# Kernel tuning notes

Measured on AMD Instinct MI355X. Metric: run time of the kernel, lower is better.

## Reference

```python
import jax, jax.numpy as jnp
import numpy as np

B, S, HID = 2, 2048, 2048
NH, HD = 16, 128
KVC, QC = 512, 1536


def _rope(x):
    # x: [B, H, S, D]; interleaved-pair rotation matching the torch view(..., D//2, 2)
    b, h, s, d = x.shape
    inv_freq = 1.0 / (10000.0 ** (jnp.arange(0, d, 2, dtype=jnp.float32) / d))  # [D/2]
    pos = jnp.arange(s, dtype=jnp.float32)
    sinusoid = pos[:, None] * inv_freq[None, :]  # [S, D/2]
    sin = jnp.sin(sinusoid)[None, None]  # [1,1,S,D/2]
    cos = jnp.cos(sinusoid)[None, None]
    xr = x.reshape(b, h, s, d // 2, 2)
    x1, x2 = xr[..., 0], xr[..., 1]
    out = jnp.stack([x1 * cos - x2 * sin, x1 * sin + x2 * cos], axis=-1)
    return out.reshape(b, h, s, d)


def setup_inputs() -> dict:
    key = jax.random.key(0)
    ks = jax.random.split(key, 14)
    def lin(k, fan_in, fan_out):
        lim = 1.0 / np.sqrt(fan_in)
        kw, kb = jax.random.split(k)
        W = jax.random.uniform(kw, (fan_in, fan_out), jnp.float32, -lim, lim)
        b = jax.random.uniform(kb, (fan_out,), jnp.float32, -lim, lim)
        return W, b
    x = jax.random.normal(ks[0], (B, S, HID), jnp.float32)
    # causal mask (positions with 0 are masked out)
    attention_mask = jnp.tril(jnp.ones((S, S), jnp.int32))[None, None]  # [1,1,S,S]
    W_dkv, b_dkv = lin(ks[1], HID, KVC)
    W_uk, b_uk = lin(ks[2], KVC, NH * HD)
    W_uv, b_uv = lin(ks[3], KVC, NH * HD)
    W_dq, b_dq = lin(ks[4], HID, QC)
    W_uq, b_uq = lin(ks[5], QC, NH * HD)
    W_o, b_o = lin(ks[6], NH * HD, HID)
    return dict(x=x, attention_mask=attention_mask,
                W_dkv=W_dkv, b_dkv=b_dkv, W_uk=W_uk, b_uk=b_uk,
                W_uv=W_uv, b_uv=b_uv, W_dq=W_dq, b_dq=b_dq,
                W_uq=W_uq, b_uq=b_uq, W_o=W_o, b_o=b_o)


def reference(x, attention_mask, W_dkv, b_dkv, W_uk, b_uk, W_uv, b_uv,
              W_dq, b_dq, W_uq, b_uq, W_o, b_o):
    b, s, _ = x.shape
    kv = x @ W_dkv + b_dkv                                   # [B,S,KVC]
    k = (kv @ W_uk + b_uk).reshape(b, s, NH, HD).transpose(0, 2, 1, 3)  # [B,H,S,D]
    v = (kv @ W_uv + b_uv).reshape(b, s, NH, HD).transpose(0, 2, 1, 3)
    q = ((x @ W_dq + b_dq) @ W_uq + b_uq).reshape(b, s, NH, HD).transpose(0, 2, 1, 3)
    q, k = _rope(q), _rope(k)
    scores = jnp.einsum('bhqd,bhkd->bhqk', q, k) / jnp.sqrt(jnp.float32(HD))
    scores = jnp.where(attention_mask == 0, jnp.float32(-1e9), scores)
    probs = jax.nn.softmax(scores, axis=-1)
    out = jnp.einsum('bhqk,bhkd->bhqd', probs, v)            # [B,H,S,D]
    out = out.transpose(0, 2, 1, 3).reshape(b, s, NH * HD)
    return out @ W_o + b_o
```

## Files before the change

### kernel.cpp

```cpp
#include <hip/hip_runtime.h>
#include <stdint.h>

typedef unsigned short u16;
typedef uint32_t u32;
typedef __attribute__((ext_vector_type(8))) short short8;
typedef __attribute__((ext_vector_type(4))) float f32x4;
typedef __attribute__((ext_vector_type(4))) u32 u32x4;
typedef __attribute__((ext_vector_type(2))) u32 u32x2;
typedef __attribute__((ext_vector_type(4))) unsigned short u16x4;

#define BS_ 4096
#define S_ 2048
#define HID_ 2048
#define KVB 32

__device__ __forceinline__ float bf2f(u16 u) { union { u32 i; float f; } v; v.i = ((u32)u) << 16; return v.f; }
__device__ __forceinline__ u16 f2bf(float f) {
  union { float f; u32 i; } v; v.f = f;
  u32 r = v.i + 0x7fffu + ((v.i >> 16) & 1u);
  return (u16)(r >> 16);
}

__device__ __forceinline__ void gload16(const void* gsrc, void* ldst) {
  __builtin_amdgcn_global_load_lds(
      (const __attribute__((address_space(1))) void*)gsrc,
      (__attribute__((address_space(3))) void*)ldst, 16, 0, 0);
}

__global__ __launch_bounds__(256) void conv_f2b(const float* __restrict__ in, u16* __restrict__ out, int n4) {
  int i = blockIdx.x * 256 + threadIdx.x;
  if (i < n4) {
    float4 v = ((const float4*)in)[i];
    u16x4 o;
    o.x = f2bf(v.x); o.y = f2bf(v.y); o.z = f2bf(v.z); o.w = f2bf(v.w);
    ((u16x4*)out)[i] = o;
  }
}

__global__ __launch_bounds__(256) void transpose_conv(const float* __restrict__ W, u16* __restrict__ WT,
                                                      int K, int N) {
  __shared__ float tile[64][65];
  const int t = threadIdx.x;
  const int kb = blockIdx.y * 64, nb = blockIdx.x * 64;
#pragma unroll
  for (int c = 0; c < 4; ++c) {
    int idx = c * 256 + t;
    int row = idx >> 4;
    int col4 = (idx & 15) * 4;
    float4 v = *(const float4*)&W[(size_t)(kb + row) * N + nb + col4];
    tile[row][col4 + 0] = v.x; tile[row][col4 + 1] = v.y;
    tile[row][col4 + 2] = v.z; tile[row][col4 + 3] = v.w;
  }
  __syncthreads();
#pragma unroll
  for (int c = 0; c < 4; ++c) {
    int idx = c * 256 + t;
    int n = idx >> 4;
    int k4 = (idx & 15) * 4;
    u16x4 o;
    o.x = f2bf(tile[k4 + 0][n]); o.y = f2bf(tile[k4 + 1][n]);
    o.z = f2bf(tile[k4 + 2][n]); o.w = f2bf(tile[k4 + 3][n]);
    *(u16x4*)&WT[(size_t)(nb + n) * K + kb + k4] = o;
  }
}

__global__ __launch_bounds__(256) void concat_bias(const float* __restrict__ b_dkv, const float* __restrict__ b_dq,
                                                   const float* __restrict__ b_uk, const float* __restrict__ b_uv,
                                                   float* __restrict__ bc1, float* __restrict__ bc2) {
  int i = blockIdx.x * 256 + threadIdx.x;
  if (i < 512) bc1[i] = b_dkv[i];
  else if (i < 2048) bc1[i] = b_dq[i - 512];
  else if (i < 4096) bc2[i - 2048] = b_uk[i - 2048];
  else if (i < 6144) bc2[i - 2048] = b_uv[i - 4096];
}

__global__ __launch_bounds__(256) void vtrans(const u16* __restrict__ KVin, u16* __restrict__ VT) {
  __shared__ u16 tile[64][136];
  const int t = threadIdx.x;
  const int st0 = blockIdx.x * 64;
  const int bh = blockIdx.y;
  const int bb = bh >> 4, h = bh & 15;
  const u16* src = KVin + (size_t)bb * S_ * 4096 + 2048 + (size_t)h * 128;
  u16* dst = VT + (size_t)bh * 128 * S_;
#pragma unroll
  for (int c = 0; c < 4; ++c) {
    int idx = c * 256 + t;
    int s = idx >> 4, ch = idx & 15;
    short8 v = *(const short8*)&src[(size_t)(st0 + s) * 4096 + ch * 8];
    *(short8*)&tile[s][ch * 8] = v;
  }
  __syncthreads();
#pragma unroll
  for (int c = 0; c < 4; ++c) {
    int idx = c * 256 + t;
    int d = idx >> 3, ch = idx & 7;
    short8 o;
#pragma unroll
    for (int j = 0; j < 8; ++j) o[j] = tile[ch * 8 + j][d];
    *(short8*)&dst[(size_t)d * S_ + st0 + ch * 8] = o;
  }
}

__global__ __launch_bounds__(256) void rope_table(float* __restrict__ cs) {
  int idx = blockIdx.x * 256 + threadIdx.x;
  int pos = idx >> 6, i = idx & 63;
  float inv = powf(10000.f, -(float)i / 64.f);
  float a = (float)pos * inv;
  cs[idx * 2] = cosf(a);
  cs[idx * 2 + 1] = sinf(a);
}

template <int OUTF32, int ROPE>
__global__ __launch_bounds__(256) void gemm_bt(const u16* __restrict__ A, int lda,
                                               const u16* __restrict__ BT,
                                               const float* __restrict__ bias,
                                               const float* __restrict__ cs,
                                               void* __restrict__ Cout,
                                               int M, int N, int K) {
  __shared__ u16 As[128 * 64];
  __shared__ u16 Bs[128 * 64];
  const int t = threadIdx.x;
  const int lane = t & 63, wave = t >> 6;
  const int wm = wave >> 1, wn = wave & 1;
  const int gx = gridDim.x;
  const int nwg = gx * gridDim.y;
  const int flat = blockIdx.y * gx + blockIdx.x;
  const int swz = (flat & 7) * (nwg >> 3) + (flat >> 3);
  const int tn = swz % gx, tm = swz / gx;
  const int r16 = lane & 15, q4 = lane >> 4;

  f32x4 acc[4][4];
#pragma unroll
  for (int m = 0; m < 4; ++m)
#pragma unroll
    for (int n = 0; n < 4; ++n) acc[m][n] = (f32x4){0.f, 0.f, 0.f, 0.f};

  for (int kt = 0; kt < K; kt += 64) {
#pragma unroll
    for (int c = 0; c < 4; ++c) {
      int idx = c * 256 + t;
      int row = idx >> 3, ch = idx & 7;
      gload16(&A[(size_t)(tm * 128 + row) * lda + kt + ch * 8], (char*)As + idx * 16);
      gload16(&BT[(size_t)(tn * 128 + row) * K + kt + ch * 8], (char*)Bs + idx * 16);
    }
    __syncthreads();
#pragma unroll
    for (int kk = 0; kk < 64; kk += 32) {
      short8 af[4], bfv[4];
#pragma unroll
      for (int m = 0; m < 4; ++m)
        af[m] = *(const short8*)&As[(wm * 64 + m * 16 + r16) * 64 + kk + q4 * 8];
#pragma unroll
      for (int n = 0; n < 4; ++n)
        bfv[n] = *(const short8*)&Bs[(wn * 64 + n * 16 + r16) * 64 + kk + q4 * 8];
      __builtin_amdgcn_s_setprio(1);
#pragma unroll
      for (int m = 0; m < 4; ++m)
#pragma unroll
        for (int n = 0; n < 4; ++n)
          acc[m][n] = __builtin_amdgcn_mfma_f32_16x16x32_bf16(bfv[n], af[m], acc[m][n], 0, 0, 0);
      __builtin_amdgcn_s_setprio(0);
    }
    __syncthreads();
  }
#pragma unroll
  for (int n = 0; n < 4; ++n) {
    int gc0 = tn * 128 + wn * 64 + n * 16 + q4 * 4;
    float4 bv4 = *(const float4*)&bias[gc0];
    const int i0 = (gc0 & 127) >> 1;
#pragma unroll
    for (int m = 0; m < 4; ++m) {
      int grow = tm * 128 + wm * 64 + m * 16 + r16;
      float v0 = acc[m][n][0] + bv4.x, v1 = acc[m][n][1] + bv4.y;
      float v2 = acc[m][n][2] + bv4.z, v3 = acc[m][n][3] + bv4.w;
      if (ROPE && gc0 < ROPE) {
        int s = grow & 2047;
        float4 cp = *(const float4*)&cs[((size_t)s * 64 + i0) * 2];
        float y0 = v0 * cp.x - v1 * cp.y;
        float y1 = v0 * cp.y + v1 * cp.x;
        float y2 = v2 * cp.z - v3 * cp.w;
        float y3 = v2 * cp.w + v3 * cp.z;
        v0 = y0; v1 = y1; v2 = y2; v3 = y3;
      }
      if (OUTF32) {
        float4 o; o.x = v0; o.y = v1; o.z = v2; o.w = v3;
        *(float4*)&((float*)Cout)[(size_t)grow * N + gc0] = o;
      } else {
        u16x4 o; o.x = f2bf(v0); o.y = f2bf(v1); o.z = f2bf(v2); o.w = f2bf(v3);
        *(u16x4*)&((u16*)Cout)[(size_t)grow * N + gc0] = o;
      }
    }
  }
}

__global__ __launch_bounds__(256, 4) void attn_kernel(const u16* __restrict__ Q, const u16* __restrict__ K,
                                                      int kld, const u16* __restrict__ VT,
                                                      u16* __restrict__ O) {
  __shared__ u16 Kl[2][KVB * 128];
  __shared__ u16 Vl[2][128 * KVB];
  __shared__ u16 Pl[4][16 * KVB];
  const int t = threadIdx.x;
  const int lane = t & 63, w = t >> 6;
  const int r16 = lane & 15, q4 = lane >> 4;
  const int b = blockIdx.x;
  const int xcd = b & 7, u = b >> 3;
  const int p = u & 15, g4 = u >> 4;
  const int bh = g4 * 8 + xcd;
  const int bb = bh >> 4, h = bh & 15;
  const u16* Qb = Q + (size_t)bb * S_ * HID_ + (size_t)h * 128;
  const u16* Kb = K + (size_t)bb * S_ * kld + (size_t)h * 128;
  const u16* VTb = VT + (size_t)bh * 128 * S_;
  u16* Ob = O + (size_t)bb * S_ * HID_ + (size_t)h * 128;

  auto stage = [&](int buf, int kvbase) {
#pragma unroll
    for (int c = 0; c < 2; ++c) {
      int s = c * 256 + t;
      int row = s >> 4;
      int chs = (s & 15) ^ (row & 7);
      gload16(&Kb[(size_t)(kvbase + row) * kld + chs * 8], (char*)Kl[buf] + s * 16);
    }
#pragma unroll
    for (int c = 0; c < 2; ++c) {
      int s = c * 256 + t;
      int row = s >> 2;
      int chs = (s & 3) ^ ((row >> 1) & 3);
      gload16(&VTb[(size_t)row * S_ + kvbase + chs * 8], (char*)Vl[buf] + s * 16);
    }
  };

  u16* Pw = &Pl[w][0];
  const float SCALE = 0.08838834764831845f;
  const int pswz = (r16 >> 1) & 3;

#pragma unroll
  for (int seg = 0; seg < 2; ++seg) {
    const int qt = seg ? (31 - p) : p;
    const int nt = 2 * qt + 2;
    const int qrow0 = qt * 64 + w * 16;
    const int q = qrow0 + r16;

    short8 qf[4];
#pragma unroll
    for (int dk = 0; dk < 4; ++dk)
      qf[dk] = *(const short8*)&Qb[(size_t)q * HID_ + dk * 32 + q4 * 8];

    f32x4 ao[8];
#pragma unroll
    for (int dn = 0; dn < 8; ++dn) ao[dn] = (f32x4){0.f, 0.f, 0.f, 0.f};
    float mr = -1e30f, lr = 0.f;

    stage(0, 0);
    __syncthreads();

    for (int ti = 0; ti < nt; ++ti) {
      const int buf = ti & 1;
      const int kv0 = ti * KVB;
      if (ti + 1 < nt) stage(buf ^ 1, kv0 + KVB);

      f32x4 sc[2];
      sc[0] = (f32x4){0.f, 0.f, 0.f, 0.f};
      sc[1] = (f32x4){0.f, 0.f, 0.f, 0.f};
#pragma unroll
      for (int dk = 0; dk < 4; ++dk) {
        short8 kf[2];
#pragma unroll
        for (int n = 0; n < 2; ++n) {
          int kr = n * 16 + r16;
          int ba = (kr * 256 + dk * 64 + q4 * 16) ^ ((kr & 7) << 4);
          kf[n] = *(const short8*)((const char*)Kl[buf] + ba);
        }
        __builtin_amdgcn_s_setprio(1);
        sc[0] = __builtin_amdgcn_mfma_f32_16x16x32_bf16(kf[0], qf[dk], sc[0], 0, 0, 0);
        sc[1] = __builtin_amdgcn_mfma_f32_16x16x32_bf16(kf[1], qf[dk], sc[1], 0, 0, 0);
        __builtin_amdgcn_s_setprio(0);
      }
      const bool nm = (kv0 + 31 > qrow0);
#pragma unroll
      for (int n = 0; n < 2; ++n)
#pragma unroll
        for (int j = 0; j < 4; ++j) {
          float sv = sc[n][j] * SCALE;
          if (nm) {
            int kv = kv0 + n * 16 + q4 * 4 + j;
            if (kv > q) sv = -1e30f;
          }
          sc[n][j] = sv;
        }
      float tm = sc[0][0];
#pragma unroll
      for (int n = 0; n < 2; ++n)
#pragma unroll
        for (int j = 0; j < 4; ++j) tm = fmaxf(tm, sc[n][j]);
      tm = fmaxf(tm, __shfl_xor(tm, 16));
      tm = fmaxf(tm, __shfl_xor(tm, 32));
      if (!__all(tm - mr <= 8.0f)) {
        float mnew = fmaxf(mr, tm);
        float fsc = __expf(mr - mnew);
        lr *= fsc; mr = mnew;
#pragma unroll
        for (int dn = 0; dn < 8; ++dn) ao[dn] *= fsc;
      }
      float ps = 0.f;
#pragma unroll
      for (int n = 0; n < 2; ++n)
#pragma unroll
        for (int j = 0; j < 4; ++j) {
          float pv = __expf(sc[n][j] - mr);
          sc[n][j] = pv;
          ps += pv;
        }
      ps += __shfl_xor(ps, 16);
      ps += __shfl_xor(ps, 32);
      lr += ps;
#pragma unroll
      for (int n = 0; n < 2; ++n) {
        u32 lo, hi;
        asm("v_cvt_pk_bf16_f32 %0, %1, %2" : "=v"(lo) : "v"(sc[n][0]), "v"(sc[n][1]));
        asm("v_cvt_pk_bf16_f32 %0, %1, %2" : "=v"(hi) : "v"(sc[n][2]), "v"(sc[n][3]));
        u32x2 pr; pr.x = lo; pr.y = hi;
        int chunk = (n * 2 + (q4 >> 1)) ^ pswz;
        int ba = r16 * 64 + chunk * 16 + (q4 & 1) * 8;
        *(u32x2*)((char*)Pw + ba) = pr;
      }
      {
        int bp = r16 * 64 + ((q4 ^ pswz) * 16);
        short8 pb = *(const short8*)((const char*)Pw + bp);
        __builtin_amdgcn_s_setprio(1);
#pragma unroll
        for (int dn = 0; dn < 8; ++dn) {
          int dr = dn * 16 + r16;
          int bv = dr * 64 + ((q4 ^ ((dr >> 1) & 3)) * 16);
          short8 vf = *(const short8*)((const char*)Vl[buf] + bv);
          ao[dn] = __builtin_amdgcn_mfma_f32_16x16x32_bf16(vf, pb, ao[dn], 0, 0, 0);
        }
        __builtin_amdgcn_s_setprio(0);
      }
      __syncthreads();
    }

    float inv = 1.f / lr;
#pragma unroll
    for (int dn = 0; dn < 8; ++dn) {
      u16x4 o;
#pragma unroll
      for (int j = 0; j < 4; ++j) o[j] = f2bf(ao[dn][j] * inv);
      *(u16x4*)&Ob[(size_t)q * HID_ + dn * 16 + q4 * 4] = o;
    }
    __syncthreads();
  }
}

extern "C" void kernel_launch(void* const* d_in, const int* in_sizes, int n_in,
                              void* d_out, int out_size, void* d_ws, size_t ws_size,
                              hipStream_t stream) {
  (void)in_sizes; (void)n_in; (void)out_size; (void)ws_size;
  const float* x     = (const float*)d_in[0];
  const float* W_dkv = (const float*)d_in[2];
  const float* b_dkv = (const float*)d_in[3];
  const float* W_uk  = (const float*)d_in[4];
  const float* b_uk  = (const float*)d_in[5];
  const float* W_uv  = (const float*)d_in[6];
  const float* b_uv  = (const float*)d_in[7];
  const float* W_dq  = (const float*)d_in[8];
  const float* b_dq  = (const float*)d_in[9];
  const float* W_uq  = (const float*)d_in[10];
  const float* b_uq  = (const float*)d_in[11];
  const float* W_o   = (const float*)d_in[12];
  const float* b_o   = (const float*)d_in[13];
  float* out = (float*)d_out;

  char* ws = (char*)d_ws;
  size_t off = 0;
  auto carve = [&](size_t bytes) { void* p = ws + off; off += (bytes + 255) & ~(size_t)255; return p; };
  u16* xb     = (u16*)carve((size_t)BS_ * 2048 * 2);
  u16* WdkvqT = (u16*)carve((size_t)2048 * 2048 * 2);
  u16* WukvT  = (u16*)carve((size_t)4096 * 512 * 2);
  u16* WuqT   = (u16*)carve((size_t)2048 * 1536 * 2);
  u16* WoT    = (u16*)carve((size_t)2048 * 2048 * 2);
  u16* kvq1   = (u16*)carve((size_t)BS_ * 2048 * 2);
  u16* kvbuf  = (u16*)carve((size_t)BS_ * 4096 * 2);
  u16* qb     = (u16*)carve((size_t)BS_ * 2048 * 2);
  u16* aob    = (u16*)carve((size_t)BS_ * 2048 * 2);
  float* cs   = (float*)carve((size_t)2048 * 64 * 2 * 4);
  float* bc1  = (float*)carve((size_t)2048 * 4);
  float* bc2  = (float*)carve((size_t)4096 * 4);
  u16* VT     = xb;

  conv_f2b<<<dim3(BS_ * 2048 / 4 / 256), 256, 0, stream>>>(x, xb, BS_ * 2048 / 4);
  transpose_conv<<<dim3(512 / 64, 2048 / 64), 256, 0, stream>>>(W_dkv, WdkvqT, 2048, 512);
  transpose_conv<<<dim3(1536 / 64, 2048 / 64), 256, 0, stream>>>(W_dq, WdkvqT + (size_t)512 * 2048, 2048, 1536);
  transpose_conv<<<dim3(2048 / 64, 512 / 64), 256, 0, stream>>>(W_uk, WukvT, 512, 2048);
  transpose_conv<<<dim3(2048 / 64, 512 / 64), 256, 0, stream>>>(W_uv, WukvT + (size_t)2048 * 512, 512, 2048);
  transpose_conv<<<dim3(2048 / 64, 1536 / 64), 256, 0, stream>>>(W_uq, WuqT, 1536, 2048);
  transpose_conv<<<dim3(2048 / 64, 2048 / 64), 256, 0, stream>>>(W_o, WoT, 2048, 2048);
  rope_table<<<dim3(512), 256, 0, stream>>>(cs);
  concat_bias<<<dim3(24), 256, 0, stream>>>(b_dkv, b_dq, b_uk, b_uv, bc1, bc2);

  gemm_bt<0, 0><<<dim3(2048 / 128, BS_ / 128), 256, 0, stream>>>(xb, 2048, WdkvqT, bc1, nullptr, kvq1, BS_, 2048, 2048);
  gemm_bt<0, 2048><<<dim3(4096 / 128, BS_ / 128), 256, 0, stream>>>(kvq1, 2048, WukvT, bc2, cs, kvbuf, BS_, 4096, 512);
  gemm_bt<0, 2048><<<dim3(2048 / 128, BS_ / 128), 256, 0, stream>>>(kvq1 + 512, 2048, WuqT, b_uq, cs, qb, BS_, 2048, 1536);

  vtrans<<<dim3(S_ / 64, 32), 256, 0, stream>>>(kvbuf, VT);

  attn_kernel<<<dim3(512), 256, 0, stream>>>(qb, kvbuf, 4096, VT, aob);

  gemm_bt<1, 0><<<dim3(2048 / 128, BS_ / 128), 256, 0, stream>>>(aob, 2048, WoT, b_o, nullptr, out, BS_, 2048, 2048);
}
```

Measured before the change: 318.1 us.

## Enlarge attention tiles to 128 query rows and 64-key KV blocks

The attention kernel now gives each wave 32 query rows (two 16-row MFMA tiles) and processes 64-key KV blocks. Each staged K/V tile is reused across twice as many queries, which halves KV loads and barriers per query. V and P LDS layouts are re-swizzled for the 64-wide blocks, and a wave skips fully masked tiles. The trade-off is half as many blocks (256 instead of 512), launch bounds of 1, and higher register and LDS pressure, so occupancy and load balance may suffer.

```diff
diff --git a/kernel.cpp b/kernel.cpp
--- a/kernel.cpp
+++ b/kernel.cpp
@@ -12,7 +12,7 @@
 #define BS_ 4096
 #define S_ 2048
 #define HID_ 2048
-#define KVB 32
+#define KVB 64
 
 __device__ __forceinline__ float bf2f(u16 u) { union { u32 i; float f; } v; v.i = ((u32)u) << 16; return v.f; }
 __device__ __forceinline__ u16 f2bf(float f) {
@@ -193,19 +193,19 @@
   }
 }
 
-__global__ __launch_bounds__(256, 4) void attn_kernel(const u16* __restrict__ Q, const u16* __restrict__ K,
+__global__ __launch_bounds__(256, 1) void attn_kernel(const u16* __restrict__ Q, const u16* __restrict__ K,
                                                       int kld, const u16* __restrict__ VT,
                                                       u16* __restrict__ O) {
   __shared__ u16 Kl[2][KVB * 128];
   __shared__ u16 Vl[2][128 * KVB];
-  __shared__ u16 Pl[4][16 * KVB];
+  __shared__ u16 Pl[4][40 * 64];
   const int t = threadIdx.x;
   const int lane = t & 63, w = t >> 6;
   const int r16 = lane & 15, q4 = lane >> 4;
   const int b = blockIdx.x;
-  const int xcd = b & 7, u = b >> 3;
-  const int p = u & 15, g4 = u >> 4;
-  const int bh = g4 * 8 + xcd;
+  const int xcd = b & 7, r = b >> 3;
+  const int p = r & 7, g = r >> 3;
+  const int bh = xcd + 8 * g;
   const int bb = bh >> 4, h = bh & 15;
   const u16* Qb = Q + (size_t)bb * S_ * HID_ + (size_t)h * 128;
   const u16* Kb = K + (size_t)bb * S_ * kld + (size_t)h * 128;
@@ -214,41 +214,45 @@
 
   auto stage = [&](int buf, int kvbase) {
 #pragma unroll
-    for (int c = 0; c < 2; ++c) {
+    for (int c = 0; c < 4; ++c) {
       int s = c * 256 + t;
       int row = s >> 4;
       int chs = (s & 15) ^ (row & 7);
       gload16(&Kb[(size_t)(kvbase + row) * kld + chs * 8], (char*)Kl[buf] + s * 16);
     }
 #pragma unroll
-    for (int c = 0; c < 2; ++c) {
+    for (int c = 0; c < 4; ++c) {
       int s = c * 256 + t;
-      int row = s >> 2;
-      int chs = (s & 3) ^ ((row >> 1) & 3);
+      int row = s >> 3;
+      int chs = (s & 7) ^ (row & 7);
       gload16(&VTb[(size_t)row * S_ + kvbase + chs * 8], (char*)Vl[buf] + s * 16);
     }
   };
 
   u16* Pw = &Pl[w][0];
   const float SCALE = 0.08838834764831845f;
-  const int pswz = (r16 >> 1) & 3;
 
 #pragma unroll
   for (int seg = 0; seg < 2; ++seg) {
-    const int qt = seg ? (31 - p) : p;
+    const int qt = seg ? (15 - p) : p;
     const int nt = 2 * qt + 2;
-    const int qrow0 = qt * 64 + w * 16;
-    const int q = qrow0 + r16;
-
-    short8 qf[4];
-#pragma unroll
-    for (int dk = 0; dk < 4; ++dk)
-      qf[dk] = *(const short8*)&Qb[(size_t)q * HID_ + dk * 32 + q4 * 8];
-
-    f32x4 ao[8];
-#pragma unroll
-    for (int dn = 0; dn < 8; ++dn) ao[dn] = (f32x4){0.f, 0.f, 0.f, 0.f};
-    float mr = -1e30f, lr = 0.f;
+    const int qrow0 = qt * 128 + w * 32;
+
+    short8 qf[2][4];
+#pragma unroll
+    for (int m = 0; m < 2; ++m)
+#pragma unroll
+      for (int dk = 0; dk < 4; ++dk)
+        qf[m][dk] = *(const short8*)&Qb[(size_t)(qrow0 + m * 16 + r16) * HID_ + dk * 32 + q4 * 8];
+
+    f32x4 ao[2][8];
+    float mr[2], lr[2];
+#pragma unroll
+    for (int m = 0; m < 2; ++m) {
+#pragma unroll
+      for (int dn = 0; dn < 8; ++dn) ao[m][dn] = (f32x4){0.f, 0.f, 0.f, 0.f};
+      mr[m] = -1e30f; lr[m] = 0.f;
+    }
 
     stage(0, 0);
     __syncthreads();
@@ -258,94 +262,129 @@
       const int kv0 = ti * KVB;
       if (ti + 1 < nt) stage(buf ^ 1, kv0 + KVB);
 
-      f32x4 sc[2];
-      sc[0] = (f32x4){0.f, 0.f, 0.f, 0.f};
-      sc[1] = (f32x4){0.f, 0.f, 0.f, 0.f};
-#pragma unroll
-      for (int dk = 0; dk < 4; ++dk) {
-        short8 kf[2];
-#pragma unroll
-        for (int n = 0; n < 2; ++n) {
-          int kr = n * 16 + r16;
-          int ba = (kr * 256 + dk * 64 + q4 * 16) ^ ((kr & 7) << 4);
-          kf[n] = *(const short8*)((const char*)Kl[buf] + ba);
-        }
-        __builtin_amdgcn_s_setprio(1);
-        sc[0] = __builtin_amdgcn_mfma_f32_16x16x32_bf16(kf[0], qf[dk], sc[0], 0, 0, 0);
-        sc[1] = __builtin_amdgcn_mfma_f32_16x16x32_bf16(kf[1], qf[dk], sc[1], 0, 0, 0);
-        __builtin_amdgcn_s_setprio(0);
-      }
-      const bool nm = (kv0 + 31 > qrow0);
-#pragma unroll
-      for (int n = 0; n < 2; ++n)
-#pragma unroll
-        for (int j = 0; j < 4; ++j) {
-          float sv = sc[n][j] * SCALE;
-          if (nm) {
-            int kv = kv0 + n * 16 + q4 * 4 + j;
-            if (kv > q) sv = -1e30f;
+      if (kv0 <= qrow0 + 31) {
+        f32x4 sc[2][4];
+#pragma unroll
+        for (int m = 0; m < 2; ++m)
+#pragma unroll
+          for (int n = 0; n < 4; ++n) sc[m][n] = (f32x4){0.f, 0.f, 0.f, 0.f};
+#pragma unroll
+        for (int dk = 0; dk < 4; ++dk) {
+          short8 kf[4];
+#pragma unroll
+          for (int n = 0; n < 4; ++n) {
+            int kr = n * 16 + r16;
+            int ba = (kr * 256 + dk * 64 + q4 * 16) ^ ((kr & 7) << 4);
+            kf[n] = *(const short8*)((const char*)Kl[buf] + ba);
           }
-          sc[n][j] = sv;
-        }
-      float tm = sc[0][0];
-#pragma unroll
-      for (int n = 0; n < 2; ++n)
-#pragma unroll
-        for (int j = 0; j < 4; ++j) tm = fmaxf(tm, sc[n][j]);
-      tm = fmaxf(tm, __shfl_xor(tm, 16));
-      tm = fmaxf(tm, __shfl_xor(tm, 32));
-      if (!__all(tm - mr <= 8.0f)) {
-        float mnew = fmaxf(mr, tm);
-        float fsc = __expf(mr - mnew);
-        lr *= fsc; mr = mnew;
-#pragma unroll
-        for (int dn = 0; dn < 8; ++dn) ao[dn] *= fsc;
-      }
-      float ps = 0.f;
-#pragma unroll
-      for (int n = 0; n < 2; ++n)
-#pragma unroll
-        for (int j = 0; j < 4; ++j) {
-          float pv = __expf(sc[n][j] - mr);
-          sc[n][j] = pv;
-          ps += pv;
-        }
-      ps += __shfl_xor(ps, 16);
-      ps += __shfl_xor(ps, 32);
-      lr += ps;
-#pragma unroll
-      for (int n = 0; n < 2; ++n) {
-        u32 lo, hi;
-        asm("v_cvt_pk_bf16_f32 %0, %1, %2" : "=v"(lo) : "v"(sc[n][0]), "v"(sc[n][1]));
-        asm("v_cvt_pk_bf16_f32 %0, %1, %2" : "=v"(hi) : "v"(sc[n][2]), "v"(sc[n][3]));
-        u32x2 pr; pr.x = lo; pr.y = hi;
-        int chunk = (n * 2 + (q4 >> 1)) ^ pswz;
-        int ba = r16 * 64 + chunk * 16 + (q4 & 1) * 8;
-        *(u32x2*)((char*)Pw + ba) = pr;
-      }
-      {
-        int bp = r16 * 64 + ((q4 ^ pswz) * 16);
-        short8 pb = *(const short8*)((const char*)Pw + bp);
-        __builtin_amdgcn_s_setprio(1);
-#pragma unroll
-        for (int dn = 0; dn < 8; ++dn) {
-          int dr = dn * 16 + r16;
-          int bv = dr * 64 + ((q4 ^ ((dr >> 1) & 3)) * 16);
-          short8 vf = *(const short8*)((const char*)Vl[buf] + bv);
-          ao[dn] = __builtin_amdgcn_mfma_f32_16x16x32_bf16(vf, pb, ao[dn], 0, 0, 0);
-        }
-        __builtin_amdgcn_s_setprio(0);
+          __builtin_amdgcn_s_setprio(1);
+#pragma unroll
+          for (int n = 0; n < 4; ++n)
+#pragma unroll
+            for (int m = 0; m < 2; ++m)
+              sc[m][n] = __builtin_amdgcn_mfma_f32_16x16x32_bf16(kf[n], qf[m][dk], sc[m][n], 0, 0, 0);
+          __builtin_amdgcn_s_setprio(0);
+        }
+        const bool nm = (kv0 + 63 > qrow0);
+#pragma unroll
+        for (int m = 0; m < 2; ++m) {
+          const int q = qrow0 + m * 16 + r16;
+#pragma unroll
+          for (int n = 0; n < 4; ++n)
+#pragma unroll
+            for (int j = 0; j < 4; ++j) {
+              float sv = sc[m][n][j] * SCALE;
+              if (nm) {
+                int kv = kv0 + n * 16 + q4 * 4 + j;
+                if (kv > q) sv = -1e30f;
+              }
+              sc[m][n][j] = sv;
+            }
+        }
+        float tm0[2];
+#pragma unroll
+        for (int m = 0; m < 2; ++m) {
+          float tm = sc[m][0][0];
+#pragma unroll
+          for (int n = 0; n < 4; ++n)
+#pragma unroll
+            for (int j = 0; j < 4; ++j) tm = fmaxf(tm, sc[m][n][j]);
+          tm = fmaxf(tm, __shfl_xor(tm, 16));
+          tm = fmaxf(tm, __shfl_xor(tm, 32));
+          tm0[m] = tm;
+        }
+        float growth = fmaxf(tm0[0] - mr[0], tm0[1] - mr[1]);
+        if (!__all(growth <= 8.0f)) {
+#pragma unroll
+          for (int m = 0; m < 2; ++m) {
+            float mnew = fmaxf(mr[m], tm0[m]);
+            float fsc = __expf(mr[m] - mnew);
+            lr[m] *= fsc; mr[m] = mnew;
+#pragma unroll
+            for (int dn = 0; dn < 8; ++dn) ao[m][dn] *= fsc;
+          }
+        }
+#pragma unroll
+        for (int m = 0; m < 2; ++m) {
+          float ps = 0.f;
+#pragma unroll
+          for (int n = 0; n < 4; ++n)
+#pragma unroll
+            for (int j = 0; j < 4; ++j) {
+              float pv = __expf(sc[m][n][j] - mr[m]);
+              sc[m][n][j] = pv;
+              ps += pv;
+            }
+          ps += __shfl_xor(ps, 16);
+          ps += __shfl_xor(ps, 32);
+          lr[m] += ps;
+        }
+#pragma unroll
+        for (int m = 0; m < 2; ++m)
+#pragma unroll
+          for (int n = 0; n < 4; ++n) {
+            u32 lo, hi;
+            asm("v_cvt_pk_bf16_f32 %0, %1, %2" : "=v"(lo) : "v"(sc[m][n][0]), "v"(sc[m][n][1]));
+            asm("v_cvt_pk_bf16_f32 %0, %1, %2" : "=v"(hi) : "v"(sc[m][n][2]), "v"(sc[m][n][3]));
+            u32x2 pr; pr.x = lo; pr.y = hi;
+            int ba = ((m * 16 + r16) * 128 + n * 32 + q4 * 8) ^ ((r16 & 7) << 4);
+            *(u32x2*)((char*)Pw + ba) = pr;
+          }
+#pragma unroll
+        for (int s = 0; s < 2; ++s) {
+          short8 pb[2];
+#pragma unroll
+          for (int m = 0; m < 2; ++m) {
+            int ba = ((m * 16 + r16) * 128 + s * 64 + q4 * 16) ^ ((r16 & 7) << 4);
+            pb[m] = *(const short8*)((const char*)Pw + ba);
+          }
+          __builtin_amdgcn_s_setprio(1);
+#pragma unroll
+          for (int dn = 0; dn < 8; ++dn) {
+            int dr = dn * 16 + r16;
+            int bv = (dr * 128 + s * 64 + q4 * 16) ^ ((dr & 7) << 4);
+            short8 vf = *(const short8*)((const char*)Vl[buf] + bv);
+#pragma unroll
+            for (int m = 0; m < 2; ++m)
+              ao[m][dn] = __builtin_amdgcn_mfma_f32_16x16x32_bf16(vf, pb[m], ao[m][dn], 0, 0, 0);
+          }
+          __builtin_amdgcn_s_setprio(0);
+        }
       }
       __syncthreads();
     }
 
-    float inv = 1.f / lr;
-#pragma unroll
-    for (int dn = 0; dn < 8; ++dn) {
-      u16x4 o;
-#pragma unroll
-      for (int j = 0; j < 4; ++j) o[j] = f2bf(ao[dn][j] * inv);
-      *(u16x4*)&Ob[(size_t)q * HID_ + dn * 16 + q4 * 4] = o;
+#pragma unroll
+    for (int m = 0; m < 2; ++m) {
+      float inv = 1.f / lr[m];
+      const int q = qrow0 + m * 16 + r16;
+#pragma unroll
+      for (int dn = 0; dn < 8; ++dn) {
+        u16x4 o;
+#pragma unroll
+        for (int j = 0; j < 4; ++j) o[j] = f2bf(ao[m][dn][j] * inv);
+        *(u16x4*)&Ob[(size_t)q * HID_ + dn * 16 + q4 * 4] = o;
+      }
     }
     __syncthreads();
   }
@@ -403,7 +442,7 @@
 
   vtrans<<<dim3(S_ / 64, 32), 256, 0, stream>>>(kvbuf, VT);
 
-  attn_kernel<<<dim3(512), 256, 0, stream>>>(qb, kvbuf, 4096, VT, aob);
+  attn_kernel<<<dim3(256), 256, 0, stream>>>(qb, kvbuf, 4096, VT, aob);
 
   gemm_bt<1, 0><<<dim3(2048 / 128, BS_ / 128), 256, 0, stream>>>(aob, 2048, WoT, b_o, nullptr, out, BS_, 2048, 2048);
 }
```

New measurement: 317.4 us. Within noise of the previous version (-0.2%).
